# Optimization experiments

Measured on AMD Instinct MI355X. Metric: run time of the kernel, lower is better.

Reference implementation:

```python
import jax, jax.numpy as jnp
import numpy as np

B, S, HS = 2, 2048, 2048
H, KVH, D = 8, 1, 256
ROPE_BASE = 10000.0


def _rope_cos_sin(position_ids, dim, base=ROPE_BASE):
    # position_ids: (B, S) int -> cos/sin: (B, S, dim)
    inv_freq = 1.0 / (base ** (jnp.arange(0, dim, 2, dtype=jnp.float32) / dim))
    thetas = position_ids.astype(jnp.float32)[..., None] * inv_freq  # (B,S,dim/2)
    emb = jnp.concatenate([thetas, thetas], axis=-1)  # (B,S,dim)
    return jnp.cos(emb), jnp.sin(emb)


def _rotate_half(x):
    x1, x2 = jnp.split(x, 2, axis=-1)
    return jnp.concatenate([-x2, x1], axis=-1)


def _apply_rope(q, k, cos, sin):
    # q,k: (B,h,S,D); cos,sin: (B,S,D) -> unsqueeze head dim
    cos = cos[:, None, :, :]
    sin = sin[:, None, :, :]
    q_emb = q * cos + _rotate_half(q) * sin
    k_emb = k * cos + _rotate_half(k) * sin
    return q_emb, k_emb


def setup_inputs() -> dict:
    key = jax.random.key(0)
    k0, k1, k2, k3, k4 = jax.random.split(key, 5)
    hidden_states = jax.random.normal(k0, (B, S, HS), jnp.float32)
    # causal additive mask: 0 where j<=i, large negative otherwise
    causal = jnp.tril(jnp.ones((S, S), dtype=bool))
    attention_mask = jnp.where(causal, 0.0, -1e9).astype(jnp.float32)
    attention_mask = jnp.broadcast_to(attention_mask[None, None], (B, 1, S, S))
    position_ids = jnp.broadcast_to(jnp.arange(S, dtype=jnp.int32)[None], (B, S))
    scale = 0.02
    Wq = jax.random.normal(k1, (HS, H * D), jnp.float32) * scale
    Wk = jax.random.normal(k2, (HS, KVH * D), jnp.float32) * scale
    Wv = jax.random.normal(k3, (HS, KVH * D), jnp.float32) * scale
    Wo = jax.random.normal(k4, (H * D, HS), jnp.float32) * scale
    return {"hidden_states": hidden_states, "attention_mask": attention_mask,
            "position_ids": position_ids, "Wq": Wq, "Wk": Wk, "Wv": Wv, "Wo": Wo}


def reference(hidden_states, attention_mask, position_ids, Wq, Wk, Wv, Wo):
    bs, seq_len, _ = hidden_states.shape
    q = (hidden_states @ Wq).reshape(bs, seq_len, H, D).transpose(0, 2, 1, 3)     # (B,H,S,D)
    k = (hidden_states @ Wk).reshape(bs, seq_len, KVH, D).transpose(0, 2, 1, 3)   # (B,KVH,S,D)
    v = (hidden_states @ Wv).reshape(bs, seq_len, KVH, D).transpose(0, 2, 1, 3)
    cos, sin = _rope_cos_sin(position_ids, D)
    q, k = _apply_rope(q, k, cos, sin)
    n_rep = H // KVH
    k = jnp.repeat(k, n_rep, axis=1)  # GQA repeat -> (B,H,S,D)
    v = jnp.repeat(v, n_rep, axis=1)
    scores = jnp.einsum('bhqd,bhkd->bhqk', q, k) / jnp.sqrt(jnp.float32(D))
    scores = scores + attention_mask
    attn = jax.nn.softmax(scores.astype(jnp.float32), axis=-1).astype(q.dtype)
    out = jnp.einsum('bhqk,bhkd->bhqd', attn, v)            # (B,H,S,D)
    out = out.transpose(0, 2, 1, 3).reshape(bs, seq_len, H * D)
    return out @ Wo
```

## Files before the change

### kernel.cpp

```cpp
#include <hip/hip_runtime.h>
#include <hip/hip_bf16.h>

typedef __bf16 bf16x8 __attribute__((ext_vector_type(8)));
typedef __bf16 bf16x4 __attribute__((ext_vector_type(4)));
typedef float  f32x4  __attribute__((ext_vector_type(4)));

#define MFMA16(a, b, c) __builtin_amdgcn_mfma_f32_16x16x32_bf16((a), (b), (c), 0, 0, 0)

#define GLOBAL_AS(p) ((const __attribute__((address_space(1))) void*)(p))
#define LDS_AS(p)    ((__attribute__((address_space(3))) void*)(p))

__global__ __launch_bounds__(256) void cvt_bf16_kernel(const float* __restrict__ in,
                                                       __bf16* __restrict__ out)
{
    const int idx = blockIdx.x * 256 + threadIdx.x;
    const float4* p = (const float4*)in + (size_t)idx * 2;
    float4 a = p[0], b = p[1];
    bf16x8 o;
    o[0] = (__bf16)a.x; o[1] = (__bf16)a.y; o[2] = (__bf16)a.z; o[3] = (__bf16)a.w;
    o[4] = (__bf16)b.x; o[5] = (__bf16)b.y; o[6] = (__bf16)b.z; o[7] = (__bf16)b.w;
    ((bf16x8*)out)[idx] = o;
}

__global__ __launch_bounds__(128) void trig_kernel(float2* __restrict__ cs)
{
    const int s = blockIdx.x, i = threadIdx.x;
    const float theta = (float)s * exp2f((float)i * (-13.287712379549449f / 128.f));
    float sn, c;
    sincosf(theta, &sn, &c);
    cs[s * 128 + i] = make_float2(c, sn);
}

__global__ __launch_bounds__(256) void transpose_cvt_kernel(const float* __restrict__ W,
                                                            __bf16* __restrict__ Bt,
                                                            int K, int N)
{
    __shared__ float t[32][33];
    const int n0 = blockIdx.x * 32, k0 = blockIdx.y * 32;
    const int x = threadIdx.x, y = threadIdx.y;
#pragma unroll
    for (int r = 0; r < 4; ++r)
        t[y + r * 8][x] = W[(size_t)(k0 + y + r * 8) * N + n0 + x];
    __syncthreads();
#pragma unroll
    for (int r = 0; r < 4; ++r)
        Bt[(size_t)(n0 + y + r * 8) * K + k0 + x] = (__bf16)t[x][y + r * 8];
}

__global__ __launch_bounds__(256) void vt_kernel(const __bf16* __restrict__ qkv,
                                                 __bf16* __restrict__ vT)
{
    __shared__ __bf16 t[32][33];
    const int s0 = blockIdx.x * 32, d0 = blockIdx.y * 32, b = blockIdx.z;
    const int x = threadIdx.x, y = threadIdx.y;
#pragma unroll
    for (int r = 0; r < 4; ++r)
        t[y + r * 8][x] = qkv[(size_t)(b * 2048 + s0 + y + r * 8) * 2560 + 2304 + d0 + x];
    __syncthreads();
#pragma unroll
    for (int r = 0; r < 4; ++r)
        vT[(size_t)(b * 256 + d0 + y + r * 8) * 2048 + s0 + x] = t[x][y + r * 8];
}

template <typename TC>
__global__ __launch_bounds__(256) void gemm_bt(const __bf16* __restrict__ A,
                                               const __bf16* __restrict__ Bt,
                                               TC* __restrict__ C,
                                               int M, int N, int K)
{
    __shared__ __bf16 As[128 * 32];
    __shared__ __bf16 Bs[128 * 32];

    const int tid  = threadIdx.x;
    const int wave = tid >> 6, lane = tid & 63;
    const int quad = lane >> 4, l16 = lane & 15;
    const int wm = (wave >> 1) * 64, wn = (wave & 1) * 64;
    const int bm = blockIdx.y * 128, bn = blockIdx.x * 128;

    f32x4 acc[4][4] = {};

    for (int k0 = 0; k0 < K; k0 += 32) {
        __syncthreads();
#pragma unroll
        for (int c = 0; c < 2; ++c) {
            const int off = tid * 16 + c * 4096;
            const int row = off >> 6;
            const int kb  = (off & 63) >> 1;
            const __bf16* ga = A  + (size_t)(bm + row) * K + k0 + kb;
            const __bf16* gb = Bt + (size_t)(bn + row) * K + k0 + kb;
            __builtin_amdgcn_global_load_lds(GLOBAL_AS(ga), LDS_AS(As + (off >> 1)), 16, 0, 0);
            __builtin_amdgcn_global_load_lds(GLOBAL_AS(gb), LDS_AS(Bs + (off >> 1)), 16, 0, 0);
        }
        __syncthreads();

        bf16x8 af[4];
#pragma unroll
        for (int mi = 0; mi < 4; ++mi)
            af[mi] = *(const bf16x8*)&As[(wm + mi * 16 + l16) * 32 + quad * 8];
#pragma unroll
        for (int ni = 0; ni < 4; ++ni) {
            bf16x8 bfr = *(const bf16x8*)&Bs[(wn + ni * 16 + l16) * 32 + quad * 8];
#pragma unroll
            for (int mi = 0; mi < 4; ++mi)
                acc[mi][ni] = MFMA16(af[mi], bfr, acc[mi][ni]);
        }
    }
#pragma unroll
    for (int mi = 0; mi < 4; ++mi)
#pragma unroll
        for (int ni = 0; ni < 4; ++ni)
#pragma unroll
            for (int r = 0; r < 4; ++r) {
                int row = bm + wm + mi * 16 + quad * 4 + r;
                int col = bn + wn + ni * 16 + l16;
                C[(size_t)row * N + col] = (TC)acc[mi][ni][r];
            }
}

__global__ __launch_bounds__(256) void rope_kernel(__bf16* __restrict__ qkv,
                                                   const float2* __restrict__ cs)
{
    const int bs = blockIdx.x;
    const int s = bs & 2047;
    const int t = threadIdx.x;
    const float QS = 0.09016843787599907f;

    const int hh = t >> 5, i0 = (t & 31) * 4;
    float2 c0 = cs[s * 128 + i0 + 0], c1 = cs[s * 128 + i0 + 1];
    float2 c2 = cs[s * 128 + i0 + 2], c3 = cs[s * 128 + i0 + 3];

    {
        __bf16* p = qkv + (size_t)bs * 2560 + hh * 256 + i0;
        bf16x4 x1 = *(const bf16x4*)p;
        bf16x4 x2 = *(const bf16x4*)(p + 128);
        bf16x4 o1, o2;
        o1[0] = (__bf16)(((float)x1[0] * c0.x - (float)x2[0] * c0.y) * QS);
        o2[0] = (__bf16)(((float)x2[0] * c0.x + (float)x1[0] * c0.y) * QS);
        o1[1] = (__bf16)(((float)x1[1] * c1.x - (float)x2[1] * c1.y) * QS);
        o2[1] = (__bf16)(((float)x2[1] * c1.x + (float)x1[1] * c1.y) * QS);
        o1[2] = (__bf16)(((float)x1[2] * c2.x - (float)x2[2] * c2.y) * QS);
        o2[2] = (__bf16)(((float)x2[2] * c2.x + (float)x1[2] * c2.y) * QS);
        o1[3] = (__bf16)(((float)x1[3] * c3.x - (float)x2[3] * c3.y) * QS);
        o2[3] = (__bf16)(((float)x2[3] * c3.x + (float)x1[3] * c3.y) * QS);
        *(bf16x4*)p = o1;
        *(bf16x4*)(p + 128) = o2;
    }
    if (t < 32) {
        const int j0 = t * 4;
        float2 d0 = cs[s * 128 + j0 + 0], d1 = cs[s * 128 + j0 + 1];
        float2 d2 = cs[s * 128 + j0 + 2], d3 = cs[s * 128 + j0 + 3];
        __bf16* p = qkv + (size_t)bs * 2560 + 2048 + j0;
        bf16x4 x1 = *(const bf16x4*)p;
        bf16x4 x2 = *(const bf16x4*)(p + 128);
        bf16x4 o1, o2;
        o1[0] = (__bf16)((float)x1[0] * d0.x - (float)x2[0] * d0.y);
        o2[0] = (__bf16)((float)x2[0] * d0.x + (float)x1[0] * d0.y);
        o1[1] = (__bf16)((float)x1[1] * d1.x - (float)x2[1] * d1.y);
        o2[1] = (__bf16)((float)x2[1] * d1.x + (float)x1[1] * d1.y);
        o1[2] = (__bf16)((float)x1[2] * d2.x - (float)x2[2] * d2.y);
        o2[2] = (__bf16)((float)x2[2] * d2.x + (float)x1[2] * d2.y);
        o1[3] = (__bf16)((float)x1[3] * d3.x - (float)x2[3] * d3.y);
        o2[3] = (__bf16)((float)x2[3] * d3.x + (float)x1[3] * d3.y);
        *(bf16x4*)p = o1;
        *(bf16x4*)(p + 128) = o2;
    }
}

__global__ __launch_bounds__(256, 2) void attn_kernel(const __bf16* __restrict__ qkv,
                                                      const __bf16* __restrict__ vTg,
                                                      __bf16* __restrict__ og)
{
    __shared__ __bf16 Ks[64 * 256];
    __shared__ __bf16 Vs[256 * 64];
    __shared__ __bf16 Ps[4][32][36];

    const int b = blockIdx.z, h = blockIdx.y;
    const int xx = (int)blockIdx.x;
    const int half = xx >> 1;
    const bool rev = ((xx & 1) == 0) ^ (b != 0);
    const int qt = rev ? 31 - half : half;
    const int q0 = qt * 64;
    const int tid  = threadIdx.x;
    const int wave = tid >> 6, lane = tid & 63;
    const int quad = lane >> 4, l16 = lane & 15;
    const int xork = l16 & 7;
    const int wm2 = wave >> 1, wn2 = wave & 1;

    bf16x8 onef;
#pragma unroll
    for (int e = 0; e < 8; ++e) onef[e] = (__bf16)1.0f;

    bf16x8 qf[2][8];
#pragma unroll
    for (int mi = 0; mi < 2; ++mi) {
        const __bf16* qptr = qkv + (size_t)(b * 2048 + q0 + wm2 * 32 + mi * 16 + l16) * 2560
                           + h * 256;
#pragma unroll
        for (int dc = 0; dc < 8; ++dc)
            qf[mi][dc] = *(const bf16x8*)(qptr + dc * 32 + quad * 8);
    }

    f32x4 oacc[2][16] = {};
    f32x4 lacc[2] = {};

    const int kKey0 = tid >> 5;
    const int kC    = (tid & 31) ^ (kKey0 & 7);
    const __bf16* kstage0 = qkv + (size_t)b * 2048 * 2560 + 2048
                          + (size_t)kKey0 * 2560 + kC * 8;
    const int vD0 = tid >> 3;
    const int vC  = (tid & 7) ^ (vD0 & 7);
    const __bf16* vstage0 = vTg + (size_t)b * 256 * 2048 + (size_t)vD0 * 2048 + vC * 8;

    int ckK[8];
#pragma unroll
    for (int dc = 0; dc < 8; ++dc) ckK[dc] = (dc * 4 + quad) ^ xork;
    const int chV = (wn2 * 4 + quad) ^ xork;

    for (int j0 = 0; j0 <= q0; j0 += 64) {
        __syncthreads();
        const __bf16* kst = kstage0 + (size_t)j0 * 2560;
        const __bf16* vst = vstage0 + j0;
#pragma unroll
        for (int p = 0; p < 8; ++p)
            __builtin_amdgcn_global_load_lds(GLOBAL_AS(kst + (size_t)p * 8 * 2560),
                                             LDS_AS(Ks + tid * 8 + p * 2048), 16, 0, 0);
#pragma unroll
        for (int p = 0; p < 8; ++p)
            __builtin_amdgcn_global_load_lds(GLOBAL_AS(vst + (size_t)p * 32 * 2048),
                                             LDS_AS(Vs + tid * 8 + p * 2048), 16, 0, 0);
        __syncthreads();

        f32x4 sc[2][2] = {};
#pragma unroll
        for (int nt = 0; nt < 2; ++nt) {
            const __bf16* krow = &Ks[(wn2 * 32 + nt * 16 + l16) * 256];
#pragma unroll
            for (int dc = 0; dc < 8; ++dc) {
                bf16x8 kf = *(const bf16x8*)(krow + ckK[dc] * 8);
                sc[0][nt] = MFMA16(qf[0][dc], kf, sc[0][nt]);
                sc[1][nt] = MFMA16(qf[1][dc], kf, sc[1][nt]);
            }
        }
        if (j0 == q0) {
#pragma unroll
            for (int nt = 0; nt < 2; ++nt) {
                int key = j0 + wn2 * 32 + nt * 16 + l16;
#pragma unroll
                for (int mi = 0; mi < 2; ++mi)
#pragma unroll
                    for (int r = 0; r < 4; ++r) {
                        int row = q0 + wm2 * 32 + mi * 16 + quad * 4 + r;
                        if (key > row) sc[mi][nt][r] = -1e30f;
                    }
            }
        }
#pragma unroll
        for (int mi = 0; mi < 2; ++mi)
#pragma unroll
            for (int nt = 0; nt < 2; ++nt)
#pragma unroll
                for (int r = 0; r < 4; ++r)
                    Ps[wave][mi * 16 + quad * 4 + r][nt * 16 + l16] =
                        (__bf16)exp2f(sc[mi][nt][r] - 8.f);
        bf16x8 pf0 = *(const bf16x8*)&Ps[wave][l16][quad * 8];
        bf16x8 pf1 = *(const bf16x8*)&Ps[wave][16 + l16][quad * 8];
#pragma unroll
        for (int dt = 0; dt < 16; ++dt) {
            const __bf16* vrow = &Vs[(dt * 16 + l16) * 64];
            bf16x8 vf = *(const bf16x8*)(vrow + chV * 8);
            oacc[0][dt] = MFMA16(pf0, vf, oacc[0][dt]);
            oacc[1][dt] = MFMA16(pf1, vf, oacc[1][dt]);
        }
        lacc[0] = MFMA16(pf0, onef, lacc[0]);
        lacc[1] = MFMA16(pf1, onef, lacc[1]);
    }

    __syncthreads();
    float* oscr = (wm2 == 0) ? (float*)Ks : (float*)Vs;
    float* lscr = (float*)Ps;
    if (wn2 == 1) {
#pragma unroll
        for (int mi = 0; mi < 2; ++mi) {
#pragma unroll
            for (int dt = 0; dt < 16; ++dt)
#pragma unroll
                for (int r = 0; r < 4; ++r)
                    oscr[(mi * 16 + quad * 4 + r) * 256 + dt * 16 + l16] = oacc[mi][dt][r];
#pragma unroll
            for (int r = 0; r < 4; ++r)
                lscr[(wm2 * 32 + mi * 16 + quad * 4 + r) * 16 + l16] = lacc[mi][r];
        }
    }
    __syncthreads();
    if (wn2 == 0) {
#pragma unroll
        for (int mi = 0; mi < 2; ++mi) {
            float invl[4];
#pragma unroll
            for (int r = 0; r < 4; ++r)
                invl[r] = 1.f / (lacc[mi][r]
                        + lscr[(wm2 * 32 + mi * 16 + quad * 4 + r) * 16 + l16]);
#pragma unroll
            for (int dt = 0; dt < 16; ++dt)
#pragma unroll
                for (int r = 0; r < 4; ++r) {
                    float o = oacc[mi][dt][r]
                            + oscr[(mi * 16 + quad * 4 + r) * 256 + dt * 16 + l16];
                    int row = q0 + wm2 * 32 + mi * 16 + quad * 4 + r;
                    int col = h * 256 + dt * 16 + l16;
                    og[(size_t)(b * 2048 + row) * 2048 + col] = (__bf16)(o * invl[r]);
                }
        }
    }
}

extern "C" void kernel_launch(void* const* d_in, const int* in_sizes, int n_in,
                              void* d_out, int out_size, void* d_ws, size_t ws_size,
                              hipStream_t stream)
{
    (void)in_sizes; (void)n_in; (void)out_size; (void)ws_size;
    const float* hidden = (const float*)d_in[0];
    const float* Wq = (const float*)d_in[3];
    const float* Wk = (const float*)d_in[4];
    const float* Wv = (const float*)d_in[5];
    const float* Wo = (const float*)d_in[6];

    char* ws = (char*)d_ws;
    __bf16* hb    = (__bf16*)(ws);
    __bf16* qkv   = (__bf16*)(ws + (16u << 20));
    __bf16* vTb   = (__bf16*)(ws + (36u << 20));
    __bf16* ob    = (__bf16*)(ws + (38u << 20));
    __bf16* Wqkvt = (__bf16*)(ws + (54u << 20));
    __bf16* Wot   = (__bf16*)(ws + (64u << 20));
    float2* csb   = (float2*)(ws + (72u << 20));
    float* out = (float*)d_out;

    dim3 blk(256);
    dim3 tblk(32, 8);
    cvt_bf16_kernel<<<dim3(4096), blk, 0, stream>>>(hidden, hb);
    trig_kernel<<<dim3(2048), dim3(128), 0, stream>>>(csb);
    transpose_cvt_kernel<<<dim3(64, 64), tblk, 0, stream>>>(Wq, Wqkvt, 2048, 2048);
    transpose_cvt_kernel<<<dim3(8, 64), tblk, 0, stream>>>(Wk, Wqkvt + (size_t)2048 * 2048, 2048, 256);
    transpose_cvt_kernel<<<dim3(8, 64), tblk, 0, stream>>>(Wv, Wqkvt + (size_t)2304 * 2048, 2048, 256);
    transpose_cvt_kernel<<<dim3(64, 64), tblk, 0, stream>>>(Wo, Wot, 2048, 2048);
    gemm_bt<__bf16><<<dim3(20, 32), blk, 0, stream>>>(hb, Wqkvt, qkv, 4096, 2560, 2048);
    rope_kernel<<<dim3(4096), blk, 0, stream>>>(qkv, csb);
    vt_kernel<<<dim3(64, 8, 2), tblk, 0, stream>>>(qkv, vTb);
    attn_kernel<<<dim3(32, 8, 2), blk, 0, stream>>>(qkv, vTb, ob);
    gemm_bt<float><<<dim3(16, 32), blk, 0, stream>>>(ob, Wot, out, 4096, 2048, 2048);
}
```

Baseline: 357.9 us.

## Pipeline K/V tile loads against compute with split barriers in attention loop

The attention loop used to load each K and V tile and then wait on full barriers before computing. Now the next K tile is prefetched into LDS right after the QK^T MFMAs finish reading Ks, and the next V tile right after the PV MFMAs finish reading Vs. Explicit vmcnt waits and s_barrier calls keep the two loads in flight across the compute phases, and s_setprio raises wave priority around the MFMA blocks. Correctness now depends on the hand-written waitcnt counts matching the eight loads issued per stage.

```diff
diff --git a/kernel.cpp b/kernel.cpp
--- a/kernel.cpp
+++ b/kernel.cpp
@@ -166,6 +166,15 @@
     }
 }
 
+static __device__ __forceinline__ void stage8(const __bf16* src, __bf16* dst,
+                                              size_t src_step)
+{
+#pragma unroll
+    for (int p = 0; p < 8; ++p)
+        __builtin_amdgcn_global_load_lds(GLOBAL_AS(src + (size_t)p * src_step),
+                                         LDS_AS(dst + p * 2048), 16, 0, 0);
+}
+
 __global__ __launch_bounds__(256, 2) void attn_kernel(const __bf16* __restrict__ qkv,
                                                       const __bf16* __restrict__ vTg,
                                                       __bf16* __restrict__ og)
@@ -210,27 +219,28 @@
     const int vD0 = tid >> 3;
     const int vC  = (tid & 7) ^ (vD0 & 7);
     const __bf16* vstage0 = vTg + (size_t)b * 256 * 2048 + (size_t)vD0 * 2048 + vC * 8;
+    __bf16* kdst = Ks + tid * 8;
+    __bf16* vdst = Vs + tid * 8;
 
     int ckK[8];
 #pragma unroll
     for (int dc = 0; dc < 8; ++dc) ckK[dc] = (dc * 4 + quad) ^ xork;
     const int chV = (wn2 * 4 + quad) ^ xork;
 
+    stage8(kstage0, kdst, (size_t)8 * 2560);
+    __builtin_amdgcn_sched_barrier(0);
+    stage8(vstage0, vdst, (size_t)32 * 2048);
+    __builtin_amdgcn_sched_barrier(0);
+
     for (int j0 = 0; j0 <= q0; j0 += 64) {
-        __syncthreads();
-        const __bf16* kst = kstage0 + (size_t)j0 * 2560;
-        const __bf16* vst = vstage0 + j0;
-#pragma unroll
-        for (int p = 0; p < 8; ++p)
-            __builtin_amdgcn_global_load_lds(GLOBAL_AS(kst + (size_t)p * 8 * 2560),
-                                             LDS_AS(Ks + tid * 8 + p * 2048), 16, 0, 0);
-#pragma unroll
-        for (int p = 0; p < 8; ++p)
-            __builtin_amdgcn_global_load_lds(GLOBAL_AS(vst + (size_t)p * 32 * 2048),
-                                             LDS_AS(Vs + tid * 8 + p * 2048), 16, 0, 0);
-        __syncthreads();
+        const bool more = (j0 + 64 <= q0);
+
+        asm volatile("s_waitcnt vmcnt(8)" ::: "memory");
+        __builtin_amdgcn_s_barrier();
+        __builtin_amdgcn_sched_barrier(0);
 
         f32x4 sc[2][2] = {};
+        __builtin_amdgcn_s_setprio(1);
 #pragma unroll
         for (int nt = 0; nt < 2; ++nt) {
             const __bf16* krow = &Ks[(wn2 * 32 + nt * 16 + l16) * 256];
@@ -241,6 +251,17 @@
                 sc[1][nt] = MFMA16(qf[1][dc], kf, sc[1][nt]);
             }
         }
+        __builtin_amdgcn_s_setprio(0);
+
+        asm volatile("s_waitcnt lgkmcnt(0)" ::: "memory");
+        __builtin_amdgcn_s_barrier();
+        __builtin_amdgcn_sched_barrier(0);
+
+        if (more) {
+            stage8(kstage0 + (size_t)(j0 + 64) * 2560, kdst, (size_t)8 * 2560);
+            __builtin_amdgcn_sched_barrier(0);
+        }
+
         if (j0 == q0) {
 #pragma unroll
             for (int nt = 0; nt < 2; ++nt) {
@@ -264,6 +285,13 @@
                         (__bf16)exp2f(sc[mi][nt][r] - 8.f);
         bf16x8 pf0 = *(const bf16x8*)&Ps[wave][l16][quad * 8];
         bf16x8 pf1 = *(const bf16x8*)&Ps[wave][16 + l16][quad * 8];
+
+        if (more) asm volatile("s_waitcnt vmcnt(8)" ::: "memory");
+        else      asm volatile("s_waitcnt vmcnt(0)" ::: "memory");
+        __builtin_amdgcn_s_barrier();
+        __builtin_amdgcn_sched_barrier(0);
+
+        __builtin_amdgcn_s_setprio(1);
 #pragma unroll
         for (int dt = 0; dt < 16; ++dt) {
             const __bf16* vrow = &Vs[(dt * 16 + l16) * 64];
@@ -273,6 +301,16 @@
         }
         lacc[0] = MFMA16(pf0, onef, lacc[0]);
         lacc[1] = MFMA16(pf1, onef, lacc[1]);
+        __builtin_amdgcn_s_setprio(0);
+
+        asm volatile("s_waitcnt lgkmcnt(0)" ::: "memory");
+        __builtin_amdgcn_s_barrier();
+        __builtin_amdgcn_sched_barrier(0);
+
+        if (more) {
+            stage8(vstage0 + (j0 + 64), vdst, (size_t)32 * 2048);
+            __builtin_amdgcn_sched_barrier(0);
+        }
     }
 
     __syncthreads();
```

Measured after the change: 355.8 us. No clear change (-0.6%).

## Pre-swizzle K and V into MFMA fragment order and load directly from global

Applied to the files above, without the earlier changes.

Adds a kernel that rearranges K into per-lane MFMA fragment order and changes the V transpose kernel to emit fragment-ordered V. The attention kernel then reads K and V fragments straight from global memory, dropping the LDS staging, both per-tile barriers and the swizzle arithmetic, and wraps the MFMA blocks in s_setprio. This removes LDS traffic and block-wide synchronisation at the cost of one extra small launch and exposed global-load latency that is no longer explicitly staged. The V buffer now reuses the region that held the hidden-state bf16 copy.

```diff
diff --git a/kernel.cpp b/kernel.cpp
--- a/kernel.cpp
+++ b/kernel.cpp
@@ -48,7 +48,7 @@
 }
 
 __global__ __launch_bounds__(256) void vt_kernel(const __bf16* __restrict__ qkv,
-                                                 __bf16* __restrict__ vT)
+                                                 __bf16* __restrict__ vf)
 {
     __shared__ __bf16 t[32][33];
     const int s0 = blockIdx.x * 32, d0 = blockIdx.y * 32, b = blockIdx.z;
@@ -57,9 +57,37 @@
     for (int r = 0; r < 4; ++r)
         t[y + r * 8][x] = qkv[(size_t)(b * 2048 + s0 + y + r * 8) * 2560 + 2304 + d0 + x];
     __syncthreads();
-#pragma unroll
-    for (int r = 0; r < 4; ++r)
-        vT[(size_t)(b * 256 + d0 + y + r * 8) * 2048 + s0 + x] = t[x][y + r * 8];
+    const int tlin = y * 32 + x;
+    if (tlin < 128) {
+        const int di = tlin & 31, ko = tlin >> 5;
+        const int d  = d0 + di;
+        const int key8 = s0 + ko * 8;
+        const int jt = key8 >> 6, wk = (key8 >> 5) & 1, quad = (key8 >> 3) & 3;
+        const int dt = d >> 4, l16 = d & 15;
+        bf16x8 u;
+#pragma unroll
+        for (int e = 0; e < 8; ++e) u[e] = t[ko * 8 + e][di];
+        size_t off = (((((size_t)b * 32 + jt) * 2 + wk) * 16 + dt) * 64
+                      + quad * 16 + l16) * 8;
+        *(bf16x8*)(vf + off) = u;
+    }
+}
+
+__global__ __launch_bounds__(256) void karr_kernel(const __bf16* __restrict__ qkv,
+                                                   __bf16* __restrict__ kf)
+{
+    const int gid = blockIdx.x * 256 + threadIdx.x;
+    const int b = gid >> 16;
+    const int r = gid & 65535;
+    const int s = r >> 5;
+    const int dc = (r >> 2) & 7;
+    const int quad = r & 3;
+    bf16x8 u = *(const bf16x8*)(qkv + (size_t)(b * 2048 + s) * 2560
+                                + 2048 + dc * 32 + quad * 8);
+    const int jt = s >> 6, nt = (s >> 4) & 3, l16 = s & 15;
+    size_t off = (((((size_t)b * 32 + jt) * 4 + nt) * 8 + dc) * 64
+                  + quad * 16 + l16) * 8;
+    *(bf16x8*)(kf + off) = u;
 }
 
 template <typename TC>
@@ -167,11 +195,11 @@
 }
 
 __global__ __launch_bounds__(256, 2) void attn_kernel(const __bf16* __restrict__ qkv,
-                                                      const __bf16* __restrict__ vTg,
+                                                      const __bf16* __restrict__ kfg,
+                                                      const __bf16* __restrict__ vfg,
                                                       __bf16* __restrict__ og)
 {
-    __shared__ __bf16 Ks[64 * 256];
-    __shared__ __bf16 Vs[256 * 64];
+    __shared__ float  Scr[2][32][256];
     __shared__ __bf16 Ps[4][32][36];
 
     const int b = blockIdx.z, h = blockIdx.y;
@@ -183,7 +211,6 @@
     const int tid  = threadIdx.x;
     const int wave = tid >> 6, lane = tid & 63;
     const int quad = lane >> 4, l16 = lane & 15;
-    const int xork = l16 & 7;
     const int wm2 = wave >> 1, wn2 = wave & 1;
 
     bf16x8 onef;
@@ -203,44 +230,23 @@
     f32x4 oacc[2][16] = {};
     f32x4 lacc[2] = {};
 
-    const int kKey0 = tid >> 5;
-    const int kC    = (tid & 31) ^ (kKey0 & 7);
-    const __bf16* kstage0 = qkv + (size_t)b * 2048 * 2560 + 2048
-                          + (size_t)kKey0 * 2560 + kC * 8;
-    const int vD0 = tid >> 3;
-    const int vC  = (tid & 7) ^ (vD0 & 7);
-    const __bf16* vstage0 = vTg + (size_t)b * 256 * 2048 + (size_t)vD0 * 2048 + vC * 8;
-
-    int ckK[8];
-#pragma unroll
-    for (int dc = 0; dc < 8; ++dc) ckK[dc] = (dc * 4 + quad) ^ xork;
-    const int chV = (wn2 * 4 + quad) ^ xork;
+    const __bf16* kf0 = kfg + (size_t)b * 524288 + (size_t)(wn2 * 2) * 4096 + lane * 8;
+    const __bf16* vf0 = vfg + (size_t)b * 524288 + (size_t)wn2 * 8192 + lane * 8;
 
     for (int j0 = 0; j0 <= q0; j0 += 64) {
-        __syncthreads();
-        const __bf16* kst = kstage0 + (size_t)j0 * 2560;
-        const __bf16* vst = vstage0 + j0;
-#pragma unroll
-        for (int p = 0; p < 8; ++p)
-            __builtin_amdgcn_global_load_lds(GLOBAL_AS(kst + (size_t)p * 8 * 2560),
-                                             LDS_AS(Ks + tid * 8 + p * 2048), 16, 0, 0);
-#pragma unroll
-        for (int p = 0; p < 8; ++p)
-            __builtin_amdgcn_global_load_lds(GLOBAL_AS(vst + (size_t)p * 32 * 2048),
-                                             LDS_AS(Vs + tid * 8 + p * 2048), 16, 0, 0);
-        __syncthreads();
-
+        const int jt = j0 >> 6;
+        const __bf16* kfp = kf0 + (size_t)jt * 16384;
         f32x4 sc[2][2] = {};
-#pragma unroll
-        for (int nt = 0; nt < 2; ++nt) {
-            const __bf16* krow = &Ks[(wn2 * 32 + nt * 16 + l16) * 256];
+        __builtin_amdgcn_s_setprio(1);
+#pragma unroll
+        for (int nt = 0; nt < 2; ++nt)
 #pragma unroll
             for (int dc = 0; dc < 8; ++dc) {
-                bf16x8 kf = *(const bf16x8*)(krow + ckK[dc] * 8);
-                sc[0][nt] = MFMA16(qf[0][dc], kf, sc[0][nt]);
-                sc[1][nt] = MFMA16(qf[1][dc], kf, sc[1][nt]);
+                bf16x8 kfr = *(const bf16x8*)(kfp + nt * 4096 + dc * 512);
+                sc[0][nt] = MFMA16(qf[0][dc], kfr, sc[0][nt]);
+                sc[1][nt] = MFMA16(qf[1][dc], kfr, sc[1][nt]);
             }
-        }
+        __builtin_amdgcn_s_setprio(0);
         if (j0 == q0) {
 #pragma unroll
             for (int nt = 0; nt < 2; ++nt) {
@@ -264,19 +270,21 @@
                         (__bf16)exp2f(sc[mi][nt][r] - 8.f);
         bf16x8 pf0 = *(const bf16x8*)&Ps[wave][l16][quad * 8];
         bf16x8 pf1 = *(const bf16x8*)&Ps[wave][16 + l16][quad * 8];
+        const __bf16* vfp = vf0 + (size_t)jt * 16384;
+        __builtin_amdgcn_s_setprio(1);
 #pragma unroll
         for (int dt = 0; dt < 16; ++dt) {
-            const __bf16* vrow = &Vs[(dt * 16 + l16) * 64];
-            bf16x8 vf = *(const bf16x8*)(vrow + chV * 8);
-            oacc[0][dt] = MFMA16(pf0, vf, oacc[0][dt]);
-            oacc[1][dt] = MFMA16(pf1, vf, oacc[1][dt]);
+            bf16x8 vfr = *(const bf16x8*)(vfp + dt * 512);
+            oacc[0][dt] = MFMA16(pf0, vfr, oacc[0][dt]);
+            oacc[1][dt] = MFMA16(pf1, vfr, oacc[1][dt]);
         }
         lacc[0] = MFMA16(pf0, onef, lacc[0]);
         lacc[1] = MFMA16(pf1, onef, lacc[1]);
+        __builtin_amdgcn_s_setprio(0);
     }
 
     __syncthreads();
-    float* oscr = (wm2 == 0) ? (float*)Ks : (float*)Vs;
+    float* oscr = &Scr[wm2][0][0];
     float* lscr = (float*)Ps;
     if (wn2 == 1) {
 #pragma unroll
@@ -327,8 +335,9 @@
 
     char* ws = (char*)d_ws;
     __bf16* hb    = (__bf16*)(ws);
+    __bf16* vfb   = (__bf16*)(ws);
     __bf16* qkv   = (__bf16*)(ws + (16u << 20));
-    __bf16* vTb   = (__bf16*)(ws + (36u << 20));
+    __bf16* kfb   = (__bf16*)(ws + (36u << 20));
     __bf16* ob    = (__bf16*)(ws + (38u << 20));
     __bf16* Wqkvt = (__bf16*)(ws + (54u << 20));
     __bf16* Wot   = (__bf16*)(ws + (64u << 20));
@@ -345,7 +354,8 @@
     transpose_cvt_kernel<<<dim3(64, 64), tblk, 0, stream>>>(Wo, Wot, 2048, 2048);
     gemm_bt<__bf16><<<dim3(20, 32), blk, 0, stream>>>(hb, Wqkvt, qkv, 4096, 2560, 2048);
     rope_kernel<<<dim3(4096), blk, 0, stream>>>(qkv, csb);
-    vt_kernel<<<dim3(64, 8, 2), tblk, 0, stream>>>(qkv, vTb);
-    attn_kernel<<<dim3(32, 8, 2), blk, 0, stream>>>(qkv, vTb, ob);
+    karr_kernel<<<dim3(512), blk, 0, stream>>>(qkv, kfb);
+    vt_kernel<<<dim3(64, 8, 2), tblk, 0, stream>>>(qkv, vfb);
+    attn_kernel<<<dim3(32, 8, 2), blk, 0, stream>>>(qkv, kfb, vfb, ob);
     gemm_bt<float><<<dim3(16, 32), blk, 0, stream>>>(ob, Wot, out, 4096, 2048, 2048);
 }
```

Result: slower. 428.4 us (+19.7%).
